# Kernel tuning notes

Hardware: AMD Instinct MI355X
Metric: run time of the kernel (lower is better)

## Reference

```python
import jax, jax.numpy as jnp
import numpy as np

K = 7          # involution kernel size
G = 16         # groups = channels // group_channels = 256 // 16
BN_EPS = 1e-3  # Keras BatchNormalization default epsilon


def setup_inputs() -> dict:
    key = jax.random.key(0)
    ks = jax.random.split(key, 6)
    B, H, W, C = 4, 56, 56, 256
    Cr = C // 4                      # reduction_ratio = 4
    x = jax.random.normal(ks[0], (B, H, W, C), dtype=jnp.float32)
    w_reduce = jax.random.normal(ks[1], (C, Cr), dtype=jnp.float32) * (1.0 / np.sqrt(C))
    gamma = jnp.ones((Cr,), dtype=jnp.float32)
    beta = jnp.zeros((Cr,), dtype=jnp.float32)
    mean = jax.random.normal(ks[2], (Cr,), dtype=jnp.float32) * 0.1
    var = jax.random.uniform(ks[3], (Cr,), dtype=jnp.float32) + 0.5
    w_span = jax.random.normal(ks[4], (Cr, K * K * G), dtype=jnp.float32) * (1.0 / np.sqrt(Cr))
    b_span = jnp.zeros((K * K * G,), dtype=jnp.float32)
    return {"x": x, "w_reduce": w_reduce, "gamma": gamma, "beta": beta,
            "mean": mean, "var": var, "w_span": w_span, "b_span": b_span}


def reference(x, w_reduce, gamma, beta, mean, var, w_span, b_span):
    B, H, W, C = x.shape
    Cg = C // G  # channels per group
    # kernel generation branch: 1x1 conv -> BN (inference) -> ReLU -> 1x1 conv
    r = jnp.einsum('bhwc,cd->bhwd', x, w_reduce)
    r = jax.nn.relu((r - mean) * (gamma / jnp.sqrt(var + BN_EPS)) + beta)
    kgen = jnp.einsum('bhwd,de->bhwe', r, w_span) + b_span      # (B,H,W,K*K*G)
    kgen = kgen.reshape(B, H, W, G, K * K)
    # im2col with SAME padding (stride=1, pad (K-1)//2 symmetric), depth order (kh, kw, C)
    p = (K - 1) // 2
    xp = jnp.pad(x, ((0, 0), (p, p), (p, p), (0, 0)))
    patches = jnp.stack([xp[:, i:i + H, j:j + W, :]
                         for i in range(K) for j in range(K)], axis=3)  # (B,H,W,K*K,C)
    patches = patches.reshape(B, H, W, K * K, G, Cg)
    # per-pixel, per-group weighted reduction over the K*K window
    out = jnp.einsum('bhwgk,bhwkgc->bhwgc', kgen, patches)
    return out.reshape(B, H, W, C)
```

## Files before the change

### kernel.cpp

```cpp
#include <hip/hip_runtime.h>
#include <hip/hip_bf16.h>
#include <stdint.h>

#define B_   4
#define H_   56
#define W_   56
#define C_   256
#define CR   64
#define G_   16
#define CG   16
#define KS   7
#define KK   49
#define PADR 3
#define NPX  (B_*H_*W_)

typedef __attribute__((ext_vector_type(8))) short bf16x8;
typedef __attribute__((ext_vector_type(4))) float f32x4;
typedef __attribute__((ext_vector_type(2))) float f32x2;

__device__ __forceinline__ uint32_t f2bf(float f) {
    uint32_t x = __float_as_uint(f);
    return (x + 0x7fffu + ((x >> 16) & 1u)) >> 16;
}
__device__ __forceinline__ uint32_t pkbf(float a, float b) {
    union { __hip_bfloat162 h; uint32_t u; } c;
    c.h = __float22bfloat162_rn(make_float2(a, b));
    return c.u;
}
__device__ __forceinline__ float blo(uint32_t w) { return __uint_as_float(w << 16); }
__device__ __forceinline__ float bhi(uint32_t w) { return __uint_as_float(w & 0xffff0000u); }

union U4V { uint4 u; bf16x8 v; };

__global__ __launch_bounds__(256) void k0_prepack(
        const float* __restrict__ wr, const float* __restrict__ wspan,
        const float* __restrict__ gamma, const float* __restrict__ beta,
        const float* __restrict__ mean, const float* __restrict__ var,
        uint16_t* __restrict__ wrp, uint16_t* __restrict__ wpp,
        float* __restrict__ scale, float* __restrict__ shift) {
    int idx = blockIdx.x * 256 + threadIdx.x;
    {
        int j = idx & 7, lane = (idx >> 3) & 63, nb = (idx >> 9) & 3,
            kb = (idx >> 11) & 1, g = idx >> 12;
        int k = kb * 32 + (lane >> 4) * 8 + j;
        int n = nb * 16 + (lane & 15);
        float v = (n < KK) ? wspan[k * (KK * G_) + g * KK + n] : 0.f;
        wpp[idx] = (uint16_t)f2bf(v);
    }
    if (idx < 16384) {
        int j = idx & 7, lane = (idx >> 3) & 63, nb = (idx >> 9) & 3, kb = idx >> 11;
        int k = kb * 32 + (lane >> 4) * 8 + j;
        int n = nb * 16 + (lane & 15);
        wrp[idx] = (uint16_t)f2bf(wr[k * CR + n]);
    }
    if (idx < CR) {
        float s = gamma[idx] * rsqrtf(var[idx] + 1e-3f);
        scale[idx] = s;
        shift[idx] = beta[idx] - mean[idx] * s;
    }
}

__global__ __launch_bounds__(256) void k1_reduce(
        const float* __restrict__ x, const uint16_t* __restrict__ wrp,
        const float* __restrict__ scale, const float* __restrict__ shift,
        uint16_t* __restrict__ r, uint16_t* __restrict__ xbf) {
    int tid = threadIdx.x;
    int lane = tid & 63, w = tid >> 6;
    int mt = blockIdx.x * 4 + w;
    int pix = mt * 16 + (lane & 15);
    int ko = (lane >> 4) * 8;
    const float* xrow = x + (size_t)pix * C_ + ko;
    f32x4 acc[4] = {{0,0,0,0},{0,0,0,0},{0,0,0,0},{0,0,0,0}};
    for (int kb = 0; kb < 8; ++kb) {
        float4 a0 = *(const float4*)(xrow + kb * 32);
        float4 a1 = *(const float4*)(xrow + kb * 32 + 4);
        U4V af;
        af.u = make_uint4(pkbf(a0.x, a0.y), pkbf(a0.z, a0.w),
                          pkbf(a1.x, a1.y), pkbf(a1.z, a1.w));
        *(uint4*)(xbf + (size_t)pix * C_ + ko + kb * 32) = af.u;
        const uint16_t* wb = wrp + kb * 2048 + lane * 8;
        #pragma unroll
        for (int nb = 0; nb < 4; ++nb) {
            bf16x8 bf_ = *(const bf16x8*)(wb + nb * 512);
            acc[nb] = __builtin_amdgcn_mfma_f32_16x16x32_bf16(af.v, bf_, acc[nb], 0, 0, 0);
        }
    }
    int rq = (lane >> 4) * 4;
    #pragma unroll
    for (int nb = 0; nb < 4; ++nb) {
        int d = nb * 16 + (lane & 15);
        float s = scale[d], sh = shift[d];
        #pragma unroll
        for (int rg = 0; rg < 4; ++rg) {
            float v = fmaf(acc[nb][rg], s, sh);
            v = v > 0.f ? v : 0.f;
            r[(size_t)(mt * 16 + rq + rg) * CR + d] = (uint16_t)f2bf(v);
        }
    }
}

#define TS   14
#define HS   20
#define XSP  21
#define KGW  56

__global__ __launch_bounds__(256, 4) void k2_involution(
        const uint16_t* __restrict__ xbf, const uint16_t* __restrict__ r,
        const uint16_t* __restrict__ wpp, const float* __restrict__ bspan,
        float* __restrict__ out) {
    __shared__ __align__(16) uint16_t xs[420 * 16];
    __shared__ __align__(16) uint16_t kg[196 * KGW];

    int tid  = threadIdx.x;
    int tile = blockIdx.x, g = blockIdx.y, b = blockIdx.z;
    int ty0 = (tile >> 2) * TS, tx0 = (tile & 3) * TS;

    #pragma unroll
    for (int pass = 0; pass < 2; ++pass) {
        int i = tid + pass * 256;
        if (i < HS * HS) {
            int py = i / HS, px = i % HS;
            int gy = ty0 + py - PADR, gx = tx0 + px - PADR;
            uint4 wA = make_uint4(0, 0, 0, 0), wB = wA;
            if (gy >= 0 && gy < H_ && gx >= 0 && gx < W_) {
                const uint16_t* xp = xbf + (((size_t)(b * H_ + gy)) * W_ + gx) * C_ + g * CG;
                wA = *(const uint4*)(xp);
                wB = *(const uint4*)(xp + 8);
            }
            uint16_t* dst = xs + (py * XSP + px) * 16;
            *(uint4*)(dst + 0) = wA;
            *(uint4*)(dst + 8) = wB;
        }
    }

    int lane = tid & 63, w = tid >> 6;
    bf16x8 bfr[2][4];
    const uint16_t* wb = wpp + g * 4096 + lane * 8;
    #pragma unroll
    for (int kb = 0; kb < 2; ++kb)
        #pragma unroll
        for (int nb = 0; nb < 4; ++nb)
            bfr[kb][nb] = *(const bf16x8*)(wb + kb * 2048 + nb * 512);
    float bias[4];
    #pragma unroll
    for (int nb = 0; nb < 4; ++nb) {
        int n = nb * 16 + (lane & 15);
        bias[nb] = (n < KK) ? bspan[g * KK + n] : 0.f;
    }
    for (int mi = 0; mi < 4; ++mi) {
        int mt = mi * 4 + w;
        if (mt < 13) {
            int m  = mt * 16 + (lane & 15);
            int mm = m < 196 ? m : 195;
            int ly = mm / TS, lx = mm % TS;
            size_t pix = ((size_t)(b * H_ + ty0 + ly)) * W_ + (tx0 + lx);
            const uint16_t* rp = r + pix * CR + (lane >> 4) * 8;
            bf16x8 a0 = *(const bf16x8*)(rp);
            bf16x8 a1 = *(const bf16x8*)(rp + 32);
            f32x4 acc[4];
            #pragma unroll
            for (int nb = 0; nb < 4; ++nb)
                acc[nb] = (f32x4){bias[nb], bias[nb], bias[nb], bias[nb]};
            #pragma unroll
            for (int nb = 0; nb < 4; ++nb) {
                acc[nb] = __builtin_amdgcn_mfma_f32_16x16x32_bf16(a0, bfr[0][nb], acc[nb], 0, 0, 0);
                acc[nb] = __builtin_amdgcn_mfma_f32_16x16x32_bf16(a1, bfr[1][nb], acc[nb], 0, 0, 0);
            }
            int row = mt * 16 + (lane >> 4) * 4;
            if (row < 196) {
                #pragma unroll
                for (int nb = 0; nb < 4; ++nb) {
                    int n = nb * 16 + (lane & 15);
                    if (n < KK) {
                        int slot = n + n / 7;
                        #pragma unroll
                        for (int rg = 0; rg < 4; ++rg) {
                            int rr  = row + rg;
                            int rho = (rr >> 1) + (rr & 1) * 98;
                            kg[rho * KGW + slot] = (uint16_t)f2bf(acc[nb][rg]);
                        }
                    }
                }
            }
        }
    }
    __syncthreads();

    if (tid < 196) {
        int p = tid >> 1, h = tid & 1;
        int ty = p / 7, tx = (p % 7) * 2;
        const uint16_t* kgL = kg + p * KGW;
        const uint16_t* kgR = kg + (98 + p) * KGW;

        f32x2 accL[4] = {{0,0},{0,0},{0,0},{0,0}};
        f32x2 accR[4] = {{0,0},{0,0},{0,0},{0,0}};
        #pragma unroll
        for (int kh = 0; kh < KS; ++kh) {
            uint4 aL = *(const uint4*)(kgL + kh * 8);
            uint4 aR = *(const uint4*)(kgR + kh * 8);
            const uint32_t kwL[4] = {aL.x, aL.y, aL.z, aL.w};
            const uint32_t kwR[4] = {aR.x, aR.y, aR.z, aR.w};
            const uint16_t* xrow = xs + ((ty + kh) * XSP + tx) * 16 + h * 8;
            #pragma unroll
            for (int j = 0; j < 8; ++j) {
                uint4 xw = *(const uint4*)(xrow + j * 16);
                float kvL = 0.f, kvR = 0.f;
                if (j < 7) kvL = (j & 1) ? bhi(kwL[j >> 1]) : blo(kwL[j >> 1]);
                if (j > 0) { int t = j - 1; kvR = (t & 1) ? bhi(kwR[t >> 1]) : blo(kwR[t >> 1]); }
                f32x2 kL = {kvL, kvL}, kR = {kvR, kvR};
                f32x2 x0 = {blo(xw.x), bhi(xw.x)};
                f32x2 x1 = {blo(xw.y), bhi(xw.y)};
                f32x2 x2 = {blo(xw.z), bhi(xw.z)};
                f32x2 x3 = {blo(xw.w), bhi(xw.w)};
                accL[0] = __builtin_elementwise_fma(kL, x0, accL[0]);
                accL[1] = __builtin_elementwise_fma(kL, x1, accL[1]);
                accL[2] = __builtin_elementwise_fma(kL, x2, accL[2]);
                accL[3] = __builtin_elementwise_fma(kL, x3, accL[3]);
                accR[0] = __builtin_elementwise_fma(kR, x0, accR[0]);
                accR[1] = __builtin_elementwise_fma(kR, x1, accR[1]);
                accR[2] = __builtin_elementwise_fma(kR, x2, accR[2]);
                accR[3] = __builtin_elementwise_fma(kR, x3, accR[3]);
            }
        }
        size_t pixL = ((size_t)(b * H_ + ty0 + ty)) * W_ + (tx0 + tx);
        float* opL = out + pixL * C_ + g * CG + h * 8;
        float* opR = opL + C_;
        *(float4*)(opL + 0) = make_float4(accL[0].x, accL[0].y, accL[1].x, accL[1].y);
        *(float4*)(opL + 4) = make_float4(accL[2].x, accL[2].y, accL[3].x, accL[3].y);
        *(float4*)(opR + 0) = make_float4(accR[0].x, accR[0].y, accR[1].x, accR[1].y);
        *(float4*)(opR + 4) = make_float4(accR[2].x, accR[2].y, accR[3].x, accR[3].y);
    }
}

extern "C" void kernel_launch(void* const* d_in, const int* in_sizes, int n_in,
                              void* d_out, int out_size, void* d_ws, size_t ws_size,
                              hipStream_t stream) {
    const float* x        = (const float*)d_in[0];
    const float* w_reduce = (const float*)d_in[1];
    const float* gamma    = (const float*)d_in[2];
    const float* beta     = (const float*)d_in[3];
    const float* mean     = (const float*)d_in[4];
    const float* var      = (const float*)d_in[5];
    const float* w_span   = (const float*)d_in[6];
    const float* b_span   = (const float*)d_in[7];
    float* out = (float*)d_out;

    uint8_t* ws = (uint8_t*)d_ws;
    uint16_t* r_ws  = (uint16_t*)(ws + 0);
    uint16_t* wrp   = (uint16_t*)(ws + 1605632);
    uint16_t* wpp   = (uint16_t*)(ws + 1638400);
    float*    scale = (float*)   (ws + 1769472);
    float*    shift = (float*)   (ws + 1769728);
    uint16_t* xbf   = (uint16_t*)(ws + 1769984);

    hipLaunchKernelGGL(k0_prepack, dim3(256), dim3(256), 0, stream,
                       w_reduce, w_span, gamma, beta, mean, var,
                       wrp, wpp, scale, shift);
    hipLaunchKernelGGL(k1_reduce, dim3(NPX / 64), dim3(256), 0, stream,
                       x, wrp, scale, shift, r_ws, xbf);
    hipLaunchKernelGGL(k2_involution, dim3(16, 16, B_), dim3(256), 0, stream,
                       xbf, r_ws, wpp, b_span, out);
}
```

Measured before the change: 98.74 us.

## Drop bf16 copy of x; convert fp32 input in involution halo load

The reduce kernel no longer writes a bf16 copy of x to the workspace. The involution kernel instead reads fp32 x directly and packs it to bf16 while filling its shared-memory halo tile. This removes a 6.4MB write and a matching bf16 read, at the price of twice the bytes per halo load in k2. The change also hoists all x loads in k1 ahead of the MFMA loop and prefetches the r operands and weights in k2 before the halo fill, which should expose more memory parallelism but raises register pressure.

```diff
diff --git a/kernel.cpp b/kernel.cpp
--- a/kernel.cpp
+++ b/kernel.cpp
@@ -63,21 +63,34 @@
 __global__ __launch_bounds__(256) void k1_reduce(
         const float* __restrict__ x, const uint16_t* __restrict__ wrp,
         const float* __restrict__ scale, const float* __restrict__ shift,
-        uint16_t* __restrict__ r, uint16_t* __restrict__ xbf) {
+        uint16_t* __restrict__ r) {
     int tid = threadIdx.x;
     int lane = tid & 63, w = tid >> 6;
     int mt = blockIdx.x * 4 + w;
     int pix = mt * 16 + (lane & 15);
     int ko = (lane >> 4) * 8;
     const float* xrow = x + (size_t)pix * C_ + ko;
+
+    float s4[4], sh4[4];
+    #pragma unroll
+    for (int nb = 0; nb < 4; ++nb) {
+        int d = nb * 16 + (lane & 15);
+        s4[nb] = scale[d];
+        sh4[nb] = shift[d];
+    }
+
+    float4 a0[8], a1[8];
+    #pragma unroll
+    for (int kb = 0; kb < 8; ++kb) {
+        a0[kb] = *(const float4*)(xrow + kb * 32);
+        a1[kb] = *(const float4*)(xrow + kb * 32 + 4);
+    }
     f32x4 acc[4] = {{0,0,0,0},{0,0,0,0},{0,0,0,0},{0,0,0,0}};
+    #pragma unroll
     for (int kb = 0; kb < 8; ++kb) {
-        float4 a0 = *(const float4*)(xrow + kb * 32);
-        float4 a1 = *(const float4*)(xrow + kb * 32 + 4);
         U4V af;
-        af.u = make_uint4(pkbf(a0.x, a0.y), pkbf(a0.z, a0.w),
-                          pkbf(a1.x, a1.y), pkbf(a1.z, a1.w));
-        *(uint4*)(xbf + (size_t)pix * C_ + ko + kb * 32) = af.u;
+        af.u = make_uint4(pkbf(a0[kb].x, a0[kb].y), pkbf(a0[kb].z, a0[kb].w),
+                          pkbf(a1[kb].x, a1[kb].y), pkbf(a1[kb].z, a1[kb].w));
         const uint16_t* wb = wrp + kb * 2048 + lane * 8;
         #pragma unroll
         for (int nb = 0; nb < 4; ++nb) {
@@ -88,13 +101,11 @@
     int rq = (lane >> 4) * 4;
     #pragma unroll
     for (int nb = 0; nb < 4; ++nb) {
-        int d = nb * 16 + (lane & 15);
-        float s = scale[d], sh = shift[d];
         #pragma unroll
         for (int rg = 0; rg < 4; ++rg) {
-            float v = fmaf(acc[nb][rg], s, sh);
+            float v = fmaf(acc[nb][rg], s4[nb], sh4[nb]);
             v = v > 0.f ? v : 0.f;
-            r[(size_t)(mt * 16 + rq + rg) * CR + d] = (uint16_t)f2bf(v);
+            r[(size_t)(mt * 16 + rq + rg) * CR + (nb * 16 + (lane & 15))] = (uint16_t)f2bf(v);
         }
     }
 }
@@ -105,7 +116,7 @@
 #define KGW  56
 
 __global__ __launch_bounds__(256, 4) void k2_involution(
-        const uint16_t* __restrict__ xbf, const uint16_t* __restrict__ r,
+        const float* __restrict__ x, const uint16_t* __restrict__ r,
         const uint16_t* __restrict__ wpp, const float* __restrict__ bspan,
         float* __restrict__ out) {
     __shared__ __align__(16) uint16_t xs[420 * 16];
@@ -114,6 +125,21 @@
     int tid  = threadIdx.x;
     int tile = blockIdx.x, g = blockIdx.y, b = blockIdx.z;
     int ty0 = (tile >> 2) * TS, tx0 = (tile & 3) * TS;
+    int lane = tid & 63, w = tid >> 6;
+
+    bf16x8 bfr[2][4];
+    const uint16_t* wb = wpp + g * 4096 + lane * 8;
+    #pragma unroll
+    for (int kb = 0; kb < 2; ++kb)
+        #pragma unroll
+        for (int nb = 0; nb < 4; ++nb)
+            bfr[kb][nb] = *(const bf16x8*)(wb + kb * 2048 + nb * 512);
+    float bias[4];
+    #pragma unroll
+    for (int nb = 0; nb < 4; ++nb) {
+        int n = nb * 16 + (lane & 15);
+        bias[nb] = (n < KK) ? bspan[g * KK + n] : 0.f;
+    }
 
     #pragma unroll
     for (int pass = 0; pass < 2; ++pass) {
@@ -123,9 +149,15 @@
             int gy = ty0 + py - PADR, gx = tx0 + px - PADR;
             uint4 wA = make_uint4(0, 0, 0, 0), wB = wA;
             if (gy >= 0 && gy < H_ && gx >= 0 && gx < W_) {
-                const uint16_t* xp = xbf + (((size_t)(b * H_ + gy)) * W_ + gx) * C_ + g * CG;
-                wA = *(const uint4*)(xp);
-                wB = *(const uint4*)(xp + 8);
+                const float* xp = x + (((size_t)(b * H_ + gy)) * W_ + gx) * C_ + g * CG;
+                float4 q0 = *(const float4*)(xp);
+                float4 q1 = *(const float4*)(xp + 4);
+                float4 q2 = *(const float4*)(xp + 8);
+                float4 q3 = *(const float4*)(xp + 12);
+                wA = make_uint4(pkbf(q0.x, q0.y), pkbf(q0.z, q0.w),
+                                pkbf(q1.x, q1.y), pkbf(q1.z, q1.w));
+                wB = make_uint4(pkbf(q2.x, q2.y), pkbf(q2.z, q2.w),
+                                pkbf(q3.x, q3.y), pkbf(q3.z, q3.w));
             }
             uint16_t* dst = xs + (py * XSP + px) * 16;
             *(uint4*)(dst + 0) = wA;
@@ -133,38 +165,31 @@
         }
     }
 
-    int lane = tid & 63, w = tid >> 6;
-    bf16x8 bfr[2][4];
-    const uint16_t* wb = wpp + g * 4096 + lane * 8;
-    #pragma unroll
-    for (int kb = 0; kb < 2; ++kb)
-        #pragma unroll
-        for (int nb = 0; nb < 4; ++nb)
-            bfr[kb][nb] = *(const bf16x8*)(wb + kb * 2048 + nb * 512);
-    float bias[4];
-    #pragma unroll
-    for (int nb = 0; nb < 4; ++nb) {
-        int n = nb * 16 + (lane & 15);
-        bias[nb] = (n < KK) ? bspan[g * KK + n] : 0.f;
-    }
+    bf16x8 ra[4][2];
+    #pragma unroll
+    for (int mi = 0; mi < 4; ++mi) {
+        int mt = mi * 4 + w;
+        int mtc = mt < 13 ? mt : 12;
+        int m  = mtc * 16 + (lane & 15);
+        int mm = m < 196 ? m : 195;
+        int ly = mm / TS, lx = mm % TS;
+        size_t pix = ((size_t)(b * H_ + ty0 + ly)) * W_ + (tx0 + lx);
+        const uint16_t* rp = r + pix * CR + (lane >> 4) * 8;
+        ra[mi][0] = *(const bf16x8*)(rp);
+        ra[mi][1] = *(const bf16x8*)(rp + 32);
+    }
+    #pragma unroll
     for (int mi = 0; mi < 4; ++mi) {
         int mt = mi * 4 + w;
         if (mt < 13) {
-            int m  = mt * 16 + (lane & 15);
-            int mm = m < 196 ? m : 195;
-            int ly = mm / TS, lx = mm % TS;
-            size_t pix = ((size_t)(b * H_ + ty0 + ly)) * W_ + (tx0 + lx);
-            const uint16_t* rp = r + pix * CR + (lane >> 4) * 8;
-            bf16x8 a0 = *(const bf16x8*)(rp);
-            bf16x8 a1 = *(const bf16x8*)(rp + 32);
             f32x4 acc[4];
             #pragma unroll
             for (int nb = 0; nb < 4; ++nb)
                 acc[nb] = (f32x4){bias[nb], bias[nb], bias[nb], bias[nb]};
             #pragma unroll
             for (int nb = 0; nb < 4; ++nb) {
-                acc[nb] = __builtin_amdgcn_mfma_f32_16x16x32_bf16(a0, bfr[0][nb], acc[nb], 0, 0, 0);
-                acc[nb] = __builtin_amdgcn_mfma_f32_16x16x32_bf16(a1, bfr[1][nb], acc[nb], 0, 0, 0);
+                acc[nb] = __builtin_amdgcn_mfma_f32_16x16x32_bf16(ra[mi][0], bfr[0][nb], acc[nb], 0, 0, 0);
+                acc[nb] = __builtin_amdgcn_mfma_f32_16x16x32_bf16(ra[mi][1], bfr[1][nb], acc[nb], 0, 0, 0);
             }
             int row = mt * 16 + (lane >> 4) * 4;
             if (row < 196) {
@@ -251,13 +276,12 @@
     uint16_t* wpp   = (uint16_t*)(ws + 1638400);
     float*    scale = (float*)   (ws + 1769472);
     float*    shift = (float*)   (ws + 1769728);
-    uint16_t* xbf   = (uint16_t*)(ws + 1769984);
 
     hipLaunchKernelGGL(k0_prepack, dim3(256), dim3(256), 0, stream,
                        w_reduce, w_span, gamma, beta, mean, var,
                        wrp, wpp, scale, shift);
     hipLaunchKernelGGL(k1_reduce, dim3(NPX / 64), dim3(256), 0, stream,
-                       x, wrp, scale, shift, r_ws, xbf);
+                       x, wrp, scale, shift, r_ws);
     hipLaunchKernelGGL(k2_involution, dim3(16, 16, B_), dim3(256), 0, stream,
-                       xbf, r_ws, wpp, b_span, out);
-}
+                       x, r_ws, wpp, b_span, out);
+}
```

Result: no change. 98.67 us (-0.1%).
